# Kernel tuning notes

Hardware: AMD Instinct MI355X
Metric: run time of the kernel (lower is better)

## Reference

```python
import jax, jax.numpy as jnp
import numpy as np

PI = float(np.pi)
DT = 0.05
N_STEPS = 5
DIFF_SCALE = 0.3


def wrap_to_pi(t):
    return (t + PI) % (2.0 * PI) - PI


def setup_inputs() -> dict:
    key = jax.random.key(0)
    ks = jax.random.split(key, 24)
    B, T, d, H, C = 1024, 256, 256, 128, 64
    s = 0.05  # generic init scale for weights
    inp = {
        "context_angles": jax.random.normal(ks[0], (B, T, d), dtype=jnp.float32),
        # Brownian increments over n_steps fixed solver steps: dW ~ N(0, dt)
        "dW": jax.random.normal(ks[1], (B, N_STEPS, d), dtype=jnp.float32) * np.sqrt(DT).astype(np.float32),
        # equinox GRUCell params: weight_ih (3H, 2d), weight_hh (3H, H), bias (3H), bias_n (H)
        "gru_wih": jax.random.normal(ks[2], (3 * H, 2 * d)) * s,
        "gru_whh": jax.random.normal(ks[3], (3 * H, H)) * s,
        "gru_b": jax.random.normal(ks[4], (3 * H,)) * s,
        "gru_bn": jax.random.normal(ks[5], (H,)) * s,
        "proj_w": jax.random.normal(ks[6], (C, H)) * s,
        "proj_b": jax.random.normal(ks[7], (C,)) * s,
        # drift MLP (depth=3): 576 -> 128 -> 128 -> 128 -> 256, last bias zeroed
        "dr_w0": jax.random.normal(ks[8], (H, 2 * d + C)) * s,
        "dr_b0": jax.random.normal(ks[9], (H,)) * s,
        "dr_w1": jax.random.normal(ks[10], (H, H)) * s,
        "dr_b1": jax.random.normal(ks[11], (H,)) * s,
        "dr_w2": jax.random.normal(ks[12], (H, H)) * s,
        "dr_b2": jax.random.normal(ks[13], (H,)) * s,
        "dr_w3": jax.random.normal(ks[14], (d, H)) * s,
        "dr_b3": jnp.zeros((d,), dtype=jnp.float32),
        # diffusion MLP (depth=2): 576 -> 128 -> 128 -> 256, last weight *0.1, bias = -2.0
        "df_w0": jax.random.normal(ks[15], (H, 2 * d + C)) * s,
        "df_b0": jax.random.normal(ks[16], (H,)) * s,
        "df_w1": jax.random.normal(ks[17], (H, H)) * s,
        "df_b1": jax.random.normal(ks[18], (H,)) * s,
        "df_w2": jax.random.normal(ks[19], (d, H)) * s * 0.1,
        "df_b2": jnp.full((d,), -2.0, dtype=jnp.float32),
    }
    return inp


def reference(context_angles, dW, gru_wih, gru_whh, gru_b, gru_bn,
              proj_w, proj_b,
              dr_w0, dr_b0, dr_w1, dr_b1, dr_w2, dr_b2, dr_w3, dr_b3,
              df_w0, df_b0, df_w1, df_b1, df_w2, df_b2):
    B, T, d = context_angles.shape
    H = gru_whh.shape[1]

    # sin/cos angle features: (B, T, 2d), scanned over time (batched GRU)
    feats = jnp.concatenate([jnp.sin(context_angles), jnp.cos(context_angles)], axis=-1)
    x_seq = jnp.swapaxes(feats, 0, 1)  # (T, B, 2d)

    def gru_step(h, x):
        gi = x @ gru_wih.T + gru_b        # (B, 3H)
        gh = h @ gru_whh.T                # (B, 3H)
        ir, iz, in_ = jnp.split(gi, 3, axis=-1)
        hr, hz, hn = jnp.split(gh, 3, axis=-1)
        r = jax.nn.sigmoid(ir + hr)
        z = jax.nn.sigmoid(iz + hz)
        n = jnp.tanh(in_ + r * (hn + gru_bn))
        h_new = n + z * (h - n)
        return h_new, None

    h0 = jnp.zeros((B, H), dtype=feats.dtype)
    h_final, _ = jax.lax.scan(gru_step, h0, x_seq)
    ctx = h_final @ proj_w.T + proj_b  # (B, ctx_dim)

    silu = jax.nn.silu

    def drift(inp):  # (B, 2d+C) -> (B, d); coeffs in identity frame of flat torus
        h = silu(inp @ dr_w0.T + dr_b0)
        h = silu(h @ dr_w1.T + dr_b1)
        h = silu(h @ dr_w2.T + dr_b2)
        return h @ dr_w3.T + dr_b3

    def diffusion_scales(inp):  # diagonal diffusion: frame = identity on flat torus
        h = silu(inp @ df_w0.T + df_b0)
        h = silu(h @ df_w1.T + df_b1)
        return jax.nn.softplus(h @ df_w2.T + df_b2) * DIFF_SCALE

    # geometric SDE integration: exp-map on flat torus = wrap(theta + v)
    theta = wrap_to_pi(context_angles[:, -1])  # (B, d)
    for k in range(N_STEPS):
        inp = jnp.concatenate([jnp.sin(theta), jnp.cos(theta), ctx], axis=-1)
        mu = drift(inp)
        sg = diffusion_scales(inp)
        theta = wrap_to_pi(theta + mu * DT + sg * dW[:, k])
    return theta
```

## Files before the change

kernel.cpp:

```cpp
#include <hip/hip_runtime.h>
#include <stdint.h>

#define PI_F      3.14159265358979323846f
#define TWO_PI_F  6.28318530717958647692f
#define DT_F      0.05f
#define DIFF_SCALE_F 0.3f

typedef short short8 __attribute__((ext_vector_type(8)));
typedef float f32x4 __attribute__((ext_vector_type(4)));
typedef float f32x2 __attribute__((ext_vector_type(2)));
typedef unsigned int u32x4 __attribute__((ext_vector_type(4)));
typedef unsigned int u32x2 __attribute__((ext_vector_type(2)));

__device__ __forceinline__ unsigned short f2bf(float x) {
    unsigned int u = __float_as_uint(x);
    u += 0x7FFFu + ((u >> 16) & 1u);
    return (unsigned short)(u >> 16);
}
__device__ __forceinline__ float bf2f(unsigned short h) {
    return __uint_as_float(((unsigned int)h) << 16);
}
__device__ __forceinline__ unsigned int cvtpk_bf16(float lo, float hi) {
    unsigned int r;
    asm("v_cvt_pk_bf16_f32 %0, %1, %2" : "=v"(r) : "v"(lo), "v"(hi));
    return r;
}
__device__ __forceinline__ float siluf(float x) {
    return x / (1.0f + __expf(-x));
}
__device__ __forceinline__ float wrapf(float t) {
    float w = fmodf(t + PI_F, TWO_PI_F);
    w = (w < 0.0f) ? w + TWO_PI_F : w;
    return w - PI_F;
}
__device__ __forceinline__ float dot4(const float* __restrict__ W, const float* __restrict__ X, int K) {
    float a = 0.0f;
#pragma unroll 4
    for (int kk = 0; kk < K; kk += 4) {
        f32x4 wv = *(const f32x4*)(W + kk);
        f32x4 xv = *(const f32x4*)(X + kk);
        a += wv[0]*xv[0] + wv[1]*xv[1] + wv[2]*xv[2] + wv[3]*xv[3];
    }
    return a;
}

#define SYNC_RAW() do { \
    asm volatile("s_waitcnt lgkmcnt(0)" ::: "memory"); \
    __builtin_amdgcn_s_barrier(); \
    __builtin_amdgcn_sched_barrier(0); \
} while (0)

__global__ void prep_kernel(const float* __restrict__ wih, const float* __restrict__ whh,
                            unsigned short* __restrict__ wihp, unsigned short* __restrict__ whhb) {
    int i = blockIdx.x * 256 + threadIdx.x;
    if (i < 196608) {
        int e = i & 7, lane = (i >> 3) & 63, rest = i >> 9;
        int ns = rest % 6, ki = (rest / 6) & 1, half = (rest / 12) & 1;
        int dt = (rest / 24) & 3, w = rest / 96;
        int col = w*96 + ns*16 + (lane & 15);
        int k   = half*256 + dt*64 + ki*32 + (lane >> 4)*8 + e;
        wihp[i] = f2bf(wih[col*512 + k]);
    }
    if (i < 384*128) whhb[i] = f2bf(whh[i]);
}

__global__ void prep2_kernel(const float* __restrict__ dr_w0, const float* __restrict__ dr_w1,
                             const float* __restrict__ dr_w2, const float* __restrict__ dr_w3,
                             const float* __restrict__ df_w0, const float* __restrict__ df_w1,
                             const float* __restrict__ df_w2,
                             unsigned short* __restrict__ dst) {
    int i = blockIdx.x * 256 + threadIdx.x;
    int e = i & 7, lane = (i >> 3) & 63;
    int l15 = lane & 15, l4 = lane >> 4;
    const float* src; int base, K, wide;
    if      (i < 73728)  { src = dr_w0; base = 0;      K = 576; wide = 0; }
    else if (i < 90112)  { src = dr_w1; base = 73728;  K = 128; wide = 0; }
    else if (i < 106496) { src = dr_w2; base = 90112;  K = 128; wide = 0; }
    else if (i < 139264) { src = dr_w3; base = 106496; K = 128; wide = 1; }
    else if (i < 212992) { src = df_w0; base = 139264; K = 576; wide = 0; }
    else if (i < 229376) { src = df_w1; base = 212992; K = 128; wide = 0; }
    else                 { src = df_w2; base = 229376; K = 128; wide = 1; }
    int lr = (i - base) >> 9;
    int nks = (K == 576) ? 18 : 4;
    int j, k;
    if (!wide) {
        int w = lr / nks, ks = lr % nks;
        j = w*16 + l15;
        k = ks*32 + l4*8 + e;
    } else {
        int ks = lr & 3, tile = (lr >> 2) & 1, w = lr >> 3;
        j = w*32 + tile*16 + l15;
        k = ks*32 + l4*8 + e;
    }
    dst[i] = f2bf(src[(size_t)j*K + k]);
}

__launch_bounds__(256, 4)
__global__ void gi_gemm_kernel(const float* __restrict__ ctx_ang,
                               const unsigned short* __restrict__ wihp,
                               unsigned int* __restrict__ P01,
                               unsigned short* __restrict__ P2) {
    __shared__ __align__(16) float ctxL[4][32*64];
    __shared__ __align__(16) unsigned short As[2][32*64];

    const int tid  = threadIdx.x;
    const int lane = tid & 63;
    const int w    = tid >> 6;
    const int l15  = lane & 15;
    const int l4   = lane >> 4;
    const int mt   = blockIdx.x;
    const int t    = mt >> 5;
    const int b0   = (mt & 31) * 32;

    const int l4r = lane >> 4;
    const int c4  = (lane & 15) * 4;

    f32x4 acc[2][6];
    const f32x4 z4 = {0.0f, 0.0f, 0.0f, 0.0f};
#pragma unroll
    for (int mi = 0; mi < 2; ++mi)
#pragma unroll
        for (int ns = 0; ns < 6; ++ns) acc[mi][ns] = z4;

#pragma unroll
    for (int dt = 0; dt < 4; ++dt) {
#pragma unroll
        for (int i = 0; i < 2; ++i) {
            const float* src = ctx_ang + ((size_t)(b0 + w*8 + i*4 + l4r) * 65536
                                          + (size_t)t * 256 + dt*64 + c4);
            void* dst = (void*)((char*)&ctxL[dt][0] + (w*8 + i*4) * 256);
            __builtin_amdgcn_global_load_lds(
                (const __attribute__((address_space(1))) unsigned int*)src,
                (__attribute__((address_space(3))) unsigned int*)dst, 16, 0, 0);
        }
    }
    asm volatile("s_waitcnt vmcnt(0)" ::: "memory");
    __builtin_amdgcn_s_barrier();
    __builtin_amdgcn_sched_barrier(0);

#pragma unroll
    for (int dt = 0; dt < 4; ++dt) {
        {
            f32x4 cv[2];
#pragma unroll
            for (int r = 0; r < 2; ++r)
                cv[r] = *(const f32x4*)((const char*)&ctxL[dt][0] + tid*16 + r*4096);
#pragma unroll
            for (int r = 0; r < 2; ++r) {
                int row = (tid >> 4) + r*16;
                int c0  = (tid & 15) * 4;
                unsigned int s01 = cvtpk_bf16(__sinf(cv[r][0]), __sinf(cv[r][1]));
                unsigned int s23 = cvtpk_bf16(__sinf(cv[r][2]), __sinf(cv[r][3]));
                unsigned int c01 = cvtpk_bf16(__cosf(cv[r][0]), __cosf(cv[r][1]));
                unsigned int c23 = cvtpk_bf16(__cosf(cv[r][2]), __cosf(cv[r][3]));
                int boff = row*128 + (((c0 >> 3) ^ (row & 7)) * 16) + (c0 & 7) * 2;
                u32x2 sv = { s01, s23 };
                u32x2 cc = { c01, c23 };
                *(u32x2*)((char*)&As[0][0] + boff) = sv;
                *(u32x2*)((char*)&As[1][0] + boff) = cc;
            }
        }
        SYNC_RAW();

#pragma unroll
        for (int half = 0; half < 2; ++half) {
            const char* Ab = (const char*)&As[half][0];
#pragma unroll
            for (int ki = 0; ki < 2; ++ki) {
                short8 aF[2], bF[6];
#pragma unroll
                for (int mi = 0; mi < 2; ++mi) {
                    int row = mi*16 + l15;
                    int kg  = ki*4 + l4;
                    aF[mi] = *(const short8*)(Ab + row*128 + ((kg ^ (row & 7)))*16);
                }
#pragma unroll
                for (int ns = 0; ns < 6; ++ns) {
                    int fidx = (((w*4 + dt)*2 + half)*2 + ki)*6 + ns;
                    bF[ns] = *(const short8*)(wihp + ((size_t)fidx*64 + lane)*8);
                }
#pragma unroll
                for (int mi = 0; mi < 2; ++mi)
#pragma unroll
                    for (int ns = 0; ns < 6; ++ns)
                        acc[mi][ns] = __builtin_amdgcn_mfma_f32_16x16x32_bf16(aF[mi], bF[ns], acc[mi][ns], 0, 0, 0);
            }
        }
        SYNC_RAW();
    }

    {
        char* stg = (char*)&ctxL[0][0];
#pragma unroll
        for (int mi = 0; mi < 2; ++mi) {
#pragma unroll
            for (int ns = 0; ns < 6; ++ns) {
                int col = w*96 + ns*16 + l15;
                int g = col >> 7, j = col & 127;
#pragma unroll
                for (int r = 0; r < 4; ++r) {
                    int b = mi*16 + l4*4 + r;
                    unsigned short vv = f2bf(acc[mi][ns][r]);
                    if (g < 2) *(unsigned short*)(stg + ((size_t)(b*128 + j))*4 + g*2) = vv;
                    else       *(unsigned short*)(stg + 16384 + ((size_t)(b*128 + j))*2) = vv;
                }
            }
        }
        SYNC_RAW();
        const u32x4* s01v = (const u32x4*)stg;
        u32x4* dst01 = (u32x4*)(P01 + ((size_t)t*1024 + b0)*128);
#pragma unroll
        for (int e = 0; e < 4; ++e)
            dst01[tid + e*256] = s01v[tid + e*256];
        const u32x4* s2v = (const u32x4*)(stg + 16384);
        u32x4* dst2 = (u32x4*)(P2 + ((size_t)t*1024 + b0)*128);
#pragma unroll
        for (int e = 0; e < 2; ++e)
            dst2[tid + e*256] = s2v[tid + e*256];
    }
}


#define LOADPF(PA, PB, tt) do { \
    if ((tt) < 256 && gw) { \
        size_t _i = ((size_t)(tt)*1024 + b0 + bb)*128 + jj0; \
        PA = *(const u32x2*)(P01 + _i); \
        PB = *(const unsigned int*)(P2 + _i); \
    } \
} while (0)

#define STEP(RDBUF, WRBUF, PA, PB, TT) do { \
    short8 aF[4]; \
    _Pragma("unroll") \
    for (int kt = 0; kt < 4; ++kt) \
        aF[kt] = *(const short8*)((const char*)(RDBUF) + l15*256 + (((kt*4 + l4) ^ (l15 & 7)))*16); \
    f32x4 a0 = z4, a1 = z4, a2 = z4; \
    _Pragma("unroll") \
    for (int kt = 0; kt < 4; ++kt) { \
        a0 = __builtin_amdgcn_mfma_f32_16x16x32_bf16(aF[kt], whB0[kt], a0, 0, 0, 0); \
        a1 = __builtin_amdgcn_mfma_f32_16x16x32_bf16(aF[kt], whB1[kt], a1, 0, 0, 0); \
        a2 = __builtin_amdgcn_mfma_f32_16x16x32_bf16(aF[kt], whB2[kt], a2, 0, 0, 0); \
    } \
    if (l4 == 0) { \
        _Pragma("unroll") \
        for (int b = 0; b < 4; ++b) { \
            ghL[(b*3 + 0)*128 + j] = a0[b]; \
            ghL[(b*3 + 1)*128 + j] = a1[b]; \
            ghL[(b*3 + 2)*128 + j] = a2[b]; \
        } \
    } \
    u32x2 _pa = PA; unsigned int _pb = PB; \
    LOADPF(PA, PB, TT); \
    SYNC_RAW(); \
    if (gw) { \
        __builtin_amdgcn_s_setprio(1); \
        f32x2 gR = *(const f32x2*)&ghL[(bb*3 + 0)*128 + jj0]; \
        f32x2 gZ = *(const f32x2*)&ghL[(bb*3 + 1)*128 + jj0]; \
        f32x2 gN = *(const f32x2*)&ghL[(bb*3 + 2)*128 + jj0]; \
        _Pragma("unroll") \
        for (int e = 0; e < 2; ++e) { \
            unsigned int pw = _pa[e]; \
            float ir  = bf2f((unsigned short)(pw & 0xFFFFu)) + bR2[e]; \
            float iz  = bf2f((unsigned short)(pw >> 16))     + bZ2[e]; \
            float in_ = bf2f((unsigned short)(_pb >> (16*e))) + bN2[e]; \
            float rg = __builtin_amdgcn_rcpf(1.0f + __expf(-(ir + gR[e]))); \
            float zg = __builtin_amdgcn_rcpf(1.0f + __expf(-(iz + gZ[e]))); \
            float ng = 1.0f - 2.0f*__builtin_amdgcn_rcpf(1.0f + __expf(2.0f*(in_ + rg*(gN[e] + bBN2[e])))); \
            H[e] = ng + zg*(H[e] - ng); \
        } \
        *(unsigned int*)((char*)(WRBUF) + bb*256 + (((jj0 >> 3) ^ bb))*16 + (jj0 & 7)*2) = cvtpk_bf16(H[0], H[1]); \
        __builtin_amdgcn_s_setprio(0); \
    } \
    SYNC_RAW(); \
} while (0)

__launch_bounds__(512, 4)
__global__ void scan_kernel(const unsigned int* __restrict__ P01,
                            const unsigned short* __restrict__ P2,
                            const unsigned short* __restrict__ whhb,
                            const float* __restrict__ gru_b,
                            const float* __restrict__ gru_bn,
                            float* __restrict__ h_ws) {
    __shared__ __align__(16) unsigned short hAbuf[2][16*128];
    __shared__ __align__(16) float ghL[4*3*128];

    const int tid  = threadIdx.x;
    const int lane = tid & 63;
    const int w    = tid >> 6;
    const int l15  = lane & 15;
    const int l4   = lane >> 4;
    const int b0   = blockIdx.x * 4;
    const int j    = w*16 + l15;
    const bool gw  = (w < 4);
    const int bb   = w;
    const int jj0  = lane * 2;

    {
        u32x4 z = {0u,0u,0u,0u};
        *(u32x4*)((char*)hAbuf + tid*16) = z;
    }

    short8 whB0[4], whB1[4], whB2[4];
#pragma unroll
    for (int kt = 0; kt < 4; ++kt) {
        whB0[kt] = *(const short8*)(whhb + (size_t)(0*128 + j)*128 + kt*32 + l4*8);
        whB1[kt] = *(const short8*)(whhb + (size_t)(1*128 + j)*128 + kt*32 + l4*8);
        whB2[kt] = *(const short8*)(whhb + (size_t)(2*128 + j)*128 + kt*32 + l4*8);
    }
    const f32x2 bR2  = *(const f32x2*)(gru_b + jj0);
    const f32x2 bZ2  = *(const f32x2*)(gru_b + 128 + jj0);
    const f32x2 bN2  = *(const f32x2*)(gru_b + 256 + jj0);
    const f32x2 bBN2 = *(const f32x2*)(gru_bn + jj0);

    float H[2] = {0.f, 0.f};
    const f32x4 z4 = {0.0f,0.0f,0.0f,0.0f};

    u32x2 PAa = {0,0}, PAb = {0,0}, PAc = {0,0}, PAd = {0,0};
    unsigned int PBa = 0, PBb = 0, PBc = 0, PBd = 0;
    LOADPF(PAa, PBa, 0);
    LOADPF(PAb, PBb, 1);
    LOADPF(PAc, PBc, 2);
    LOADPF(PAd, PBd, 3);
    __syncthreads();

    for (int t = 0; t < 256; t += 4) {
        STEP(&hAbuf[0][0], &hAbuf[1][0], PAa, PBa, t + 4);
        STEP(&hAbuf[1][0], &hAbuf[0][0], PAb, PBb, t + 5);
        STEP(&hAbuf[0][0], &hAbuf[1][0], PAc, PBc, t + 6);
        STEP(&hAbuf[1][0], &hAbuf[0][0], PAd, PBd, t + 7);
    }

    if (gw) {
        f32x2 hv = { H[0], H[1] };
        *(f32x2*)(h_ws + (size_t)(b0 + bb)*128 + jj0) = hv;
    }
}

#define AFRAG(BUF, S, ks) (*(const short8*)((const char*)(BUF) + l15*(S) + ((((ks)*4 + l4) ^ (l15 & 7))*16)))
#define PF18(W, ks) (*(const short8*)((W) + (((size_t)(w*18 + (ks)))*64 + lane)*8))
#define PF4(W, ks)  (*(const short8*)((W) + (((size_t)(w*4 + (ks)))*64 + lane)*8))
#define PFW(W, tile, ks) (*(const short8*)((W) + (((size_t)((w*2 + (tile))*4 + (ks)))*64 + lane)*8))
#define HSTORE(BUF, bb, col, val) (*(unsigned short*)((char*)(BUF) + (bb)*256 + ((((col)>>3) ^ ((bb)&7))*16) + ((col)&7)*2) = f2bf(val))
#define MFMA16(af, bf, c) __builtin_amdgcn_mfma_f32_16x16x32_bf16((af), (bf), (c), 0, 0, 0)

__launch_bounds__(512, 1)
__global__ void sde_kernel(const float* __restrict__ ctx_ang,
                           const float* __restrict__ dW,
                           const float* __restrict__ proj_w,
                           const float* __restrict__ proj_b,
                           const float* __restrict__ dr_b0, const float* __restrict__ dr_b1,
                           const float* __restrict__ dr_b2, const float* __restrict__ dr_b3,
                           const float* __restrict__ df_b0, const float* __restrict__ df_b1,
                           const float* __restrict__ df_b2,
                           const unsigned short* __restrict__ W0d, const unsigned short* __restrict__ W1d,
                           const unsigned short* __restrict__ W2d, const unsigned short* __restrict__ W3d,
                           const unsigned short* __restrict__ W0f, const unsigned short* __restrict__ W1f,
                           const unsigned short* __restrict__ W2f,
                           const float* __restrict__ h_ws,
                           float* __restrict__ out) {
    __shared__ __align__(16) float th[4*256];
    __shared__ __align__(16) float ctxs[4*64];
    __shared__ __align__(16) float h32[4*128];
    __shared__ __align__(16) unsigned short inpA[16*576];
    __shared__ __align__(16) unsigned short hA[16*128], hB[16*128], hC[16*128], hD[16*128];

    const int tid  = threadIdx.x;
    const int lane = tid & 63;
    const int w    = tid >> 6;
    const int l15  = lane & 15;
    const int l4   = lane >> 4;
    const int b0   = blockIdx.x * 4;
    const f32x4 z4 = {0.f,0.f,0.f,0.f};

    if (tid < 512) h32[tid & 511] = 0.0f;
    h32[tid] = 0.0f;
    __syncthreads();
    {
        ((float*)h32)[tid] = h_ws[(size_t)b0*128 + tid];
    }
    __syncthreads();
    if (tid < 256) {
        int b = tid >> 6, c = tid & 63;
        ctxs[tid] = proj_b[c] + dot4(proj_w + (size_t)c*128, h32 + b*128, 128);
    }
#pragma unroll
    for (int e = 0; e < 2; ++e) {
        int idx = tid + e*512; int b = idx >> 8, i = idx & 255;
        th[idx] = wrapf(ctx_ang[((size_t)(b0 + b)*256 + 255)*256 + i]);
    }

    const int j  = w*16 + l15;
    const int j20 = w*32 + l15;
    const int j21 = w*32 + 16 + l15;
    const float bd0 = dr_b0[j], bd1 = dr_b1[j], bd2 = dr_b2[j];
    const float bf0 = df_b0[j], bf1 = df_b1[j];
    const float bd3t0 = dr_b3[j20], bd3t1 = dr_b3[j21];
    const float bf2t0 = df_b2[j20], bf2t1 = df_b2[j21];
    __syncthreads();

    for (int k = 0; k < 5; ++k) {
#pragma unroll
        for (int e = 0; e < 5; ++e) {
            int idx = tid + e*512;
            if (idx < 2304) {
                int b = idx / 576;
                int i = idx - b*576;
                float vv;
                if (i < 256)      vv = __sinf(th[(b<<8) + i]);
                else if (i < 512) vv = __cosf(th[(b<<8) + i - 256]);
                else              vv = ctxs[(b<<6) + i - 512];
                *(unsigned short*)((char*)inpA + b*1152 + (((i>>3) ^ (b&7))*16) + (i&7)*2) = f2bf(vv);
            }
        }
        __syncthreads();

        {
            f32x4 a0=z4,a1=z4,c0=z4,c1=z4;
#pragma unroll
            for (int ks = 0; ks < 18; ks += 2) {
                short8 af0 = AFRAG(inpA, 1152, ks);
                short8 af1 = AFRAG(inpA, 1152, ks+1);
                a0 = MFMA16(af0, PF18(W0d, ks),   a0);
                c0 = MFMA16(af0, PF18(W0f, ks),   c0);
                a1 = MFMA16(af1, PF18(W0d, ks+1), a1);
                c1 = MFMA16(af1, PF18(W0f, ks+1), c1);
            }
#pragma unroll
            for (int r = 0; r < 4; ++r) {
                int bb = l4*4 + r;
                HSTORE(hA, bb, j, siluf(a0[r] + a1[r] + bd0));
                HSTORE(hC, bb, j, siluf(c0[r] + c1[r] + bf0));
            }
        }
        __syncthreads();

        {
            f32x4 a0=z4,a1=z4,c0=z4,c1=z4;
#pragma unroll
            for (int ks = 0; ks < 4; ks += 2) {
                short8 aA0 = AFRAG(hA, 256, ks), aA1 = AFRAG(hA, 256, ks+1);
                short8 aC0 = AFRAG(hC, 256, ks), aC1 = AFRAG(hC, 256, ks+1);
                a0 = MFMA16(aA0, PF4(W1d, ks),   a0);
                c0 = MFMA16(aC0, PF4(W1f, ks),   c0);
                a1 = MFMA16(aA1, PF4(W1d, ks+1), a1);
                c1 = MFMA16(aC1, PF4(W1f, ks+1), c1);
            }
#pragma unroll
            for (int r = 0; r < 4; ++r) {
                int bb = l4*4 + r;
                HSTORE(hB, bb, j, siluf(a0[r] + a1[r] + bd1));
                HSTORE(hD, bb, j, siluf(c0[r] + c1[r] + bf1));
            }
        }
        __syncthreads();

        float sgr[2][4];
        {
            f32x4 a0=z4,a1=z4,s0=z4,s1=z4,s2=z4,s3=z4;
#pragma unroll
            for (int ks = 0; ks < 4; ks += 2) {
                short8 b0f = AFRAG(hB, 256, ks), b1f = AFRAG(hB, 256, ks+1);
                short8 d0f = AFRAG(hD, 256, ks), d1f = AFRAG(hD, 256, ks+1);
                a0 = MFMA16(b0f, PF4(W2d, ks),   a0);
                a1 = MFMA16(b1f, PF4(W2d, ks+1), a1);
                s0 = MFMA16(d0f, PFW(W2f, 0, ks),   s0);
                s1 = MFMA16(d1f, PFW(W2f, 0, ks+1), s1);
                s2 = MFMA16(d0f, PFW(W2f, 1, ks),   s2);
                s3 = MFMA16(d1f, PFW(W2f, 1, ks+1), s3);
            }
#pragma unroll
            for (int r = 0; r < 4; ++r) {
                int bb = l4*4 + r;
                HSTORE(hA, bb, j, siluf(a0[r] + a1[r] + bd2));
                float aa0 = s0[r] + s1[r] + bf2t0;
                float aa1 = s2[r] + s3[r] + bf2t1;
                float sp0 = (aa0 > 15.f) ? aa0 : log1pf(__expf(aa0));
                float sp1 = (aa1 > 15.f) ? aa1 : log1pf(__expf(aa1));
                sgr[0][r] = sp0 * DIFF_SCALE_F;
                sgr[1][r] = sp1 * DIFF_SCALE_F;
            }
        }
        __syncthreads();

        {
            f32x4 m0=z4,m1=z4,m2=z4,m3=z4;
#pragma unroll
            for (int ks = 0; ks < 4; ks += 2) {
                short8 h0f = AFRAG(hA, 256, ks), h1f = AFRAG(hA, 256, ks+1);
                m0 = MFMA16(h0f, PFW(W3d, 0, ks),   m0);
                m1 = MFMA16(h1f, PFW(W3d, 0, ks+1), m1);
                m2 = MFMA16(h0f, PFW(W3d, 1, ks),   m2);
                m3 = MFMA16(h1f, PFW(W3d, 1, ks+1), m3);
            }
            if (l4 == 0) {
#pragma unroll
                for (int r = 0; r < 4; ++r) {
                    int bb = r;
                    {
                        float mu = m0[r] + m1[r] + bd3t0;
                        float dw = dW[((size_t)(b0 + bb)*5 + k)*256 + j20];
                        th[(bb<<8) + j20] = wrapf(th[(bb<<8) + j20] + mu*DT_F + sgr[0][r]*dw);
                    }
                    {
                        float mu = m2[r] + m3[r] + bd3t1;
                        float dw = dW[((size_t)(b0 + bb)*5 + k)*256 + j21];
                        th[(bb<<8) + j21] = wrapf(th[(bb<<8) + j21] + mu*DT_F + sgr[1][r]*dw);
                    }
                }
            }
        }
        __syncthreads();
    }

#pragma unroll
    for (int e = 0; e < 2; ++e) {
        int idx = tid + e*512;
        out[(size_t)b0*256 + idx] = th[idx];
    }
}

extern "C" void kernel_launch(void* const* d_in, const int* in_sizes, int n_in,
                              void* d_out, int out_size, void* d_ws, size_t ws_size,
                              hipStream_t stream) {
    const float* ctx_ang = (const float*)d_in[0];
    const float* dW      = (const float*)d_in[1];
    const float* wih     = (const float*)d_in[2];
    const float* whh     = (const float*)d_in[3];
    const float* gru_b   = (const float*)d_in[4];
    const float* gru_bn  = (const float*)d_in[5];
    const float* proj_w  = (const float*)d_in[6];
    const float* proj_b  = (const float*)d_in[7];
    const float* dr_w0   = (const float*)d_in[8];
    const float* dr_b0   = (const float*)d_in[9];
    const float* dr_w1   = (const float*)d_in[10];
    const float* dr_b1   = (const float*)d_in[11];
    const float* dr_w2   = (const float*)d_in[12];
    const float* dr_b2   = (const float*)d_in[13];
    const float* dr_w3   = (const float*)d_in[14];
    const float* dr_b3   = (const float*)d_in[15];
    const float* df_w0   = (const float*)d_in[16];
    const float* df_b0   = (const float*)d_in[17];
    const float* df_w1   = (const float*)d_in[18];
    const float* df_b1   = (const float*)d_in[19];
    const float* df_w2   = (const float*)d_in[20];
    const float* df_b2   = (const float*)d_in[21];
    float* out = (float*)d_out;

    char* ws = (char*)d_ws;
    unsigned int*   P01  = (unsigned int*)ws;
    unsigned short* P2   = (unsigned short*)(ws + 134217728);
    unsigned short* wihp = (unsigned short*)(ws + 201326592);
    unsigned short* whhb = (unsigned short*)(ws + 201719808);
    float*          h_ws = (float*)(ws + 201818112);

    unsigned short* Wb  = (unsigned short*)ws;
    unsigned short* W0d = Wb;
    unsigned short* W1d = Wb + 73728;
    unsigned short* W2d = Wb + 90112;
    unsigned short* W3d = Wb + 106496;
    unsigned short* W0f = Wb + 139264;
    unsigned short* W1f = Wb + 212992;
    unsigned short* W2f = Wb + 229376;

    prep_kernel<<<768, 256, 0, stream>>>(wih, whh, wihp, whhb);
    gi_gemm_kernel<<<8192, 256, 0, stream>>>(ctx_ang, wihp, P01, P2);
    scan_kernel<<<256, 512, 0, stream>>>(P01, P2, whhb, gru_b, gru_bn, h_ws);
    prep2_kernel<<<1024, 256, 0, stream>>>(dr_w0, dr_w1, dr_w2, dr_w3, df_w0, df_w1, df_w2, Wb);
    sde_kernel<<<256, 512, 0, stream>>>(ctx_ang, dW,
        proj_w, proj_b, dr_b0, dr_b1, dr_b2, dr_b3, df_b0, df_b1, df_b2,
        W0d, W1d, W2d, W3d, W0f, W1f, W2f, h_ws, out);
}
```

Measured before the change: 446.9 us.

## Compute GRU gates directly from MFMA accumulators, removing LDS exchange and barrier

The batch rows of the recurrent state are now placed at A-matrix rows 0, 4, 8 and 12. Each lane can then read its own batch's gate pre-activations from the first MFMA accumulator element, so all eight waves update one hidden element each from registers. This drops the per-step shared-memory staging of gate values and one of the two block barriers per time step on the serial 256-step recurrence. The cost is that every wave now runs the transcendental gate math, and the input projection loads become scalar per lane. Small cleanups in the SDE kernel prologue are included.

```diff
diff --git a/kernel.cpp b/kernel.cpp
--- a/kernel.cpp
+++ b/kernel.cpp
@@ -222,10 +222,10 @@
 
 
 #define LOADPF(PA, PB, tt) do { \
-    if ((tt) < 256 && gw) { \
-        size_t _i = ((size_t)(tt)*1024 + b0 + bb)*128 + jj0; \
-        PA = *(const u32x2*)(P01 + _i); \
-        PB = *(const unsigned int*)(P2 + _i); \
+    if ((tt) < 256) { \
+        size_t _i = ((size_t)(tt)*1024 + b0 + l4)*128 + j; \
+        PA = P01[_i]; \
+        PB = P2[_i]; \
     } \
 } while (0)
 
@@ -241,35 +241,18 @@
         a1 = __builtin_amdgcn_mfma_f32_16x16x32_bf16(aF[kt], whB1[kt], a1, 0, 0, 0); \
         a2 = __builtin_amdgcn_mfma_f32_16x16x32_bf16(aF[kt], whB2[kt], a2, 0, 0, 0); \
     } \
-    if (l4 == 0) { \
-        _Pragma("unroll") \
-        for (int b = 0; b < 4; ++b) { \
-            ghL[(b*3 + 0)*128 + j] = a0[b]; \
-            ghL[(b*3 + 1)*128 + j] = a1[b]; \
-            ghL[(b*3 + 2)*128 + j] = a2[b]; \
-        } \
-    } \
-    u32x2 _pa = PA; unsigned int _pb = PB; \
+    unsigned int _pa = PA; unsigned short _pb = PB; \
     LOADPF(PA, PB, TT); \
-    SYNC_RAW(); \
-    if (gw) { \
-        __builtin_amdgcn_s_setprio(1); \
-        f32x2 gR = *(const f32x2*)&ghL[(bb*3 + 0)*128 + jj0]; \
-        f32x2 gZ = *(const f32x2*)&ghL[(bb*3 + 1)*128 + jj0]; \
-        f32x2 gN = *(const f32x2*)&ghL[(bb*3 + 2)*128 + jj0]; \
-        _Pragma("unroll") \
-        for (int e = 0; e < 2; ++e) { \
-            unsigned int pw = _pa[e]; \
-            float ir  = bf2f((unsigned short)(pw & 0xFFFFu)) + bR2[e]; \
-            float iz  = bf2f((unsigned short)(pw >> 16))     + bZ2[e]; \
-            float in_ = bf2f((unsigned short)(_pb >> (16*e))) + bN2[e]; \
-            float rg = __builtin_amdgcn_rcpf(1.0f + __expf(-(ir + gR[e]))); \
-            float zg = __builtin_amdgcn_rcpf(1.0f + __expf(-(iz + gZ[e]))); \
-            float ng = 1.0f - 2.0f*__builtin_amdgcn_rcpf(1.0f + __expf(2.0f*(in_ + rg*(gN[e] + bBN2[e])))); \
-            H[e] = ng + zg*(H[e] - ng); \
-        } \
-        *(unsigned int*)((char*)(WRBUF) + bb*256 + (((jj0 >> 3) ^ bb))*16 + (jj0 & 7)*2) = cvtpk_bf16(H[0], H[1]); \
-        __builtin_amdgcn_s_setprio(0); \
+    { \
+        float ir  = bf2f((unsigned short)(_pa & 0xFFFFu)) + bR; \
+        float iz  = bf2f((unsigned short)(_pa >> 16))     + bZ; \
+        float in_ = bf2f(_pb)                             + bN; \
+        float rg = __builtin_amdgcn_rcpf(1.0f + __expf(-(ir + a0[0]))); \
+        float zg = __builtin_amdgcn_rcpf(1.0f + __expf(-(iz + a1[0]))); \
+        float ng = 1.0f - 2.0f*__builtin_amdgcn_rcpf(1.0f + __expf(2.0f*(in_ + rg*(a2[0] + bBN)))); \
+        H = ng + zg*(H - ng); \
+        int row = l4*4; \
+        *(unsigned short*)((char*)(WRBUF) + row*256 + (((j >> 3) ^ (row & 7))*16) + (j & 7)*2) = f2bf(H); \
     } \
     SYNC_RAW(); \
 } while (0)
@@ -282,7 +265,6 @@
                             const float* __restrict__ gru_bn,
                             float* __restrict__ h_ws) {
     __shared__ __align__(16) unsigned short hAbuf[2][16*128];
-    __shared__ __align__(16) float ghL[4*3*128];
 
     const int tid  = threadIdx.x;
     const int lane = tid & 63;
@@ -291,9 +273,6 @@
     const int l4   = lane >> 4;
     const int b0   = blockIdx.x * 4;
     const int j    = w*16 + l15;
-    const bool gw  = (w < 4);
-    const int bb   = w;
-    const int jj0  = lane * 2;
 
     {
         u32x4 z = {0u,0u,0u,0u};
@@ -307,16 +286,16 @@
         whB1[kt] = *(const short8*)(whhb + (size_t)(1*128 + j)*128 + kt*32 + l4*8);
         whB2[kt] = *(const short8*)(whhb + (size_t)(2*128 + j)*128 + kt*32 + l4*8);
     }
-    const f32x2 bR2  = *(const f32x2*)(gru_b + jj0);
-    const f32x2 bZ2  = *(const f32x2*)(gru_b + 128 + jj0);
-    const f32x2 bN2  = *(const f32x2*)(gru_b + 256 + jj0);
-    const f32x2 bBN2 = *(const f32x2*)(gru_bn + jj0);
-
-    float H[2] = {0.f, 0.f};
+    const float bR  = gru_b[j];
+    const float bZ  = gru_b[128 + j];
+    const float bN  = gru_b[256 + j];
+    const float bBN = gru_bn[j];
+
+    float H = 0.f;
     const f32x4 z4 = {0.0f,0.0f,0.0f,0.0f};
 
-    u32x2 PAa = {0,0}, PAb = {0,0}, PAc = {0,0}, PAd = {0,0};
-    unsigned int PBa = 0, PBb = 0, PBc = 0, PBd = 0;
+    unsigned int  PAa = 0, PAb = 0, PAc = 0, PAd = 0;
+    unsigned short PBa = 0, PBb = 0, PBc = 0, PBd = 0;
     LOADPF(PAa, PBa, 0);
     LOADPF(PAb, PBb, 1);
     LOADPF(PAc, PBc, 2);
@@ -330,10 +309,7 @@
         STEP(&hAbuf[1][0], &hAbuf[0][0], PAd, PBd, t + 7);
     }
 
-    if (gw) {
-        f32x2 hv = { H[0], H[1] };
-        *(f32x2*)(h_ws + (size_t)(b0 + bb)*128 + jj0) = hv;
-    }
+    h_ws[(size_t)(b0 + l4)*128 + j] = H;
 }
 
 #define AFRAG(BUF, S, ks) (*(const short8*)((const char*)(BUF) + l15*(S) + ((((ks)*4 + l4) ^ (l15 & 7))*16)))
@@ -372,12 +348,9 @@
     const int b0   = blockIdx.x * 4;
     const f32x4 z4 = {0.f,0.f,0.f,0.f};
 
-    if (tid < 512) h32[tid & 511] = 0.0f;
-    h32[tid] = 0.0f;
+    h32[tid & 511] = 0.0f;
     __syncthreads();
-    {
-        ((float*)h32)[tid] = h_ws[(size_t)b0*128 + tid];
-    }
+    ((float*)h32)[tid] = h_ws[(size_t)b0*128 + tid];
     __syncthreads();
     if (tid < 256) {
         int b = tid >> 6, c = tid & 63;
```

Measured after the change: 399.1 us (median of 2 runs). 10.7% less time.
